# Kernel tuning notes

Measured on AMD Instinct MI355X. Metric: run time of the kernel, lower is better.

The kernel has to match this reference:

```python
import jax, jax.numpy as jnp
import numpy as np

N_NODES = 50000
N_EDGES = 800000
QRY = 128
KEY = 128
VAL = 128
HEADS = 8
HEAD_FEATS = VAL // HEADS
BN_EPS = 1e-5


def setup_inputs() -> dict:
    key = jax.random.key(0)
    ks = jax.random.split(key, 12)
    inp = {
        "ft_q": jax.random.normal(ks[0], (N_NODES, QRY), dtype=jnp.float32),
        "ft_k": jax.random.normal(ks[1], (N_NODES, KEY), dtype=jnp.float32),
        "src": jax.random.randint(ks[2], (N_EDGES,), 0, N_NODES, dtype=jnp.int32),
        "dst": jax.random.randint(ks[3], (N_EDGES,), 0, N_NODES, dtype=jnp.int32),
        # learned params
        "Wq": jax.random.normal(ks[4], (VAL, QRY), dtype=jnp.float32) / np.sqrt(QRY),
        "bq": jnp.zeros((VAL,), dtype=jnp.float32),
        "Wk": jax.random.normal(ks[5], (VAL, KEY), dtype=jnp.float32) / np.sqrt(KEY),
        "Wv": jax.random.normal(ks[6], (VAL, QRY), dtype=jnp.float32) / np.sqrt(QRY),
        "attn_e": jax.random.normal(ks[7], (VAL,), dtype=jnp.float32),
        "bn_q_g": jnp.ones((QRY,), dtype=jnp.float32),
        "bn_q_b": jnp.zeros((QRY,), dtype=jnp.float32),
        "bn_k_g": jnp.ones((KEY,), dtype=jnp.float32),
        "bn_k_b": jnp.zeros((KEY,), dtype=jnp.float32),
    }
    return inp


def _batch_norm(x, gamma, beta):
    # training-mode BatchNorm1d: normalize over batch dim
    mean = jnp.mean(x, axis=0, keepdims=True)
    var = jnp.var(x, axis=0, keepdims=True)
    return (x - mean) * jax.lax.rsqrt(var + BN_EPS) * gamma + beta


def reference(ft_q, ft_k, src, dst, Wq, bq, Wk, Wv, attn_e,
              bn_q_g, bn_q_b, bn_k_g, bn_k_b):
    ft_q = _batch_norm(ft_q, bn_q_g, bn_q_b)
    ft_k = _batch_norm(ft_k, bn_k_g, bn_k_b)

    q = ft_q @ Wq.T + bq                      # [N, VAL]
    k = ft_k @ Wk.T                           # [N, VAL]
    v = (ft_q @ Wv.T).reshape(-1, HEADS, HEAD_FEATS)  # [N, H, D]

    # u_add_v: per-edge e = q[src] + k[dst]
    e = q[src] + k[dst]                       # [E, VAL]
    e = (attn_e * jax.nn.sigmoid(e)).reshape(-1, HEADS, HEAD_FEATS).sum(-1)  # [E, H]

    # edge_softmax grouped by destination node
    m = jax.ops.segment_max(e, dst, num_segments=N_NODES)   # [N, H]
    ex = jnp.exp(e - m[dst])                                # [E, H]
    s = jax.ops.segment_sum(ex, dst, num_segments=N_NODES)  # [N, H]
    a = ex / s[dst]                                         # [E, H]

    # u_mul_e_sum: scatter-sum of v[src] * a over destination
    msg = v[src] * a[:, :, None]                            # [E, H, D]
    rst = jax.ops.segment_sum(msg, dst, num_segments=N_NODES)  # [N, H, D]
    return rst.reshape(-1, VAL)
```

## Files before the change

kernel.cpp:

```cpp
#include <hip/hip_runtime.h>

#define N_NODES 50000
#define N_EDGES 800000
#define FEATS 128
#define NCHUNK 196
#define CPAD 50176
#define GEMM_BX 196
#define GEMM_BLOCKS 392
#define SCAT_BLOCKS 3125
#define NTILE 782
#define NF_WAVES 8192
#define STAT_BLOCKS 256
#define HIST_BLOCKS 512

typedef __attribute__((ext_vector_type(8))) short bf16x8;
typedef __attribute__((ext_vector_type(4))) float f32x4;
typedef union { uint4 u; bf16x8 v; } pack8;

__device__ __forceinline__ unsigned short f2bf(float f){
  unsigned u = __float_as_uint(f);
  u += 0x7FFF + ((u >> 16) & 1);
  return (unsigned short)(u >> 16);
}
__device__ __forceinline__ unsigned cvtpk(float lo, float hi){
  unsigned r;
  asm("v_cvt_pk_bf16_f32 %0, %1, %2" : "=v"(r) : "v"(lo), "v"(hi));
  return r;
}
__device__ __forceinline__ void unpack8(uint4 p, float* f){
  f[0]=__uint_as_float(p.x << 16); f[1]=__uint_as_float(p.x & 0xffff0000u);
  f[2]=__uint_as_float(p.y << 16); f[3]=__uint_as_float(p.y & 0xffff0000u);
  f[4]=__uint_as_float(p.z << 16); f[5]=__uint_as_float(p.z & 0xffff0000u);
  f[6]=__uint_as_float(p.w << 16); f[7]=__uint_as_float(p.w & 0xffff0000u);
}

__global__ __launch_bounds__(256) void stats_hist_kernel(
    const float* __restrict__ ftq, const float* __restrict__ ftk,
    float* __restrict__ sums, const int* __restrict__ dstE,
    int* __restrict__ counts, int* __restrict__ csums,
    unsigned short* __restrict__ rankE, unsigned short* __restrict__ xqb){
  __shared__ float red[4*FEATS];
  __shared__ int lchunk[NCHUNK];
  int tid = threadIdx.x, bid = blockIdx.x;
  if (bid < STAT_BLOCKS){
    for (int i = tid; i < 4*FEATS; i += 256) red[i] = 0.f;
    __syncthreads();
    int sub = tid >> 5, c4 = tid & 31;
    const float* Xs = (sub < 4) ? ftq : ftk;
    int so = (sub < 4) ? 0 : 2*FEATS;
    bool isq = (sub < 4);
    float a0=0,a1=0,a2=0,a3=0,b0=0,b1=0,b2=0,b3=0;
    #pragma unroll 4
    for (int r = bid*4 + (sub&3); r < N_NODES; r += STAT_BLOCKS*4){
      float4 x = *(const float4*)(Xs + (size_t)r*FEATS + c4*4);
      if (isq)
        *(uint2*)&xqb[(size_t)r*FEATS + c4*4] = make_uint2(cvtpk(x.x,x.y), cvtpk(x.z,x.w));
      a0+=x.x; b0+=x.x*x.x; a1+=x.y; b1+=x.y*x.y;
      a2+=x.z; b2+=x.z*x.z; a3+=x.w; b3+=x.w*x.w;
    }
    a0 += __shfl_xor(a0,32); a1 += __shfl_xor(a1,32);
    a2 += __shfl_xor(a2,32); a3 += __shfl_xor(a3,32);
    b0 += __shfl_xor(b0,32); b1 += __shfl_xor(b1,32);
    b2 += __shfl_xor(b2,32); b3 += __shfl_xor(b3,32);
    if ((tid & 63) < 32){
      int c0 = c4*4;
      atomicAdd(&red[so + c0+0], a0); atomicAdd(&red[so + c0+1], a1);
      atomicAdd(&red[so + c0+2], a2); atomicAdd(&red[so + c0+3], a3);
      atomicAdd(&red[so + FEATS + c0+0], b0); atomicAdd(&red[so + FEATS + c0+1], b1);
      atomicAdd(&red[so + FEATS + c0+2], b2); atomicAdd(&red[so + FEATS + c0+3], b3);
    }
    __syncthreads();
    for (int i = tid; i < 4*FEATS; i += 256) atomicAdd(&sums[i], red[i]);
  } else {
    for (int i = tid; i < NCHUNK; i += 256) lchunk[i] = 0;
    __syncthreads();
    for (int t = (bid-STAT_BLOCKS)*256 + tid; t < N_EDGES; t += HIST_BLOCKS*256){
      int d = dstE[t];
      int p = atomicAdd(&counts[d], 1);
      rankE[t] = (unsigned short)p;
      atomicAdd(&lchunk[d >> 8], 1);
    }
    __syncthreads();
    for (int i = tid; i < NCHUNK; i += 256)
      if (lchunk[i]) atomicAdd(&csums[i], lchunk[i]);
  }
}

__global__ __launch_bounds__(256) void scan_fold_kernel(
    const int* __restrict__ counts, const int* __restrict__ csums,
    int* __restrict__ loc, int* __restrict__ bscan,
    const float* __restrict__ Wq, const float* __restrict__ bq,
    const float* __restrict__ Wk, const float* __restrict__ Wv,
    const float* __restrict__ gq, const float* __restrict__ bqn,
    const float* __restrict__ gk, const float* __restrict__ bkn,
    const float* __restrict__ sums,
    unsigned short* __restrict__ Wb, float* __restrict__ bias){
  __shared__ int s[256];
  int tid = threadIdx.x, bid = blockIdx.x;
  if (bid < NCHUNK){
    int i = bid*256 + tid;
    int v = counts[i];
    s[tid] = v; __syncthreads();
    for (int d = 1; d < 256; d <<= 1){
      int tv = (tid >= d) ? s[tid-d] : 0; __syncthreads();
      s[tid] += tv; __syncthreads();
    }
    loc[i] = s[tid] - v;
  } else if (bid == NCHUNK){
    int v = (tid < NCHUNK) ? csums[tid] : 0;
    s[tid] = v; __syncthreads();
    for (int d = 1; d < 256; d <<= 1){
      int tv = (tid >= d) ? s[tid-d] : 0; __syncthreads();
      s[tid] += tv; __syncthreads();
    }
    if (tid < NCHUNK) bscan[tid] = s[tid] - v;
  } else {
    int wv = (bid - NCHUNK - 1)*4 + (tid >> 6);
    int lane = tid & 63;
    int m = wv >> 7;
    int o = wv & 127;
    const float* Wsrc = (m==0) ? Wq : (m==1) ? Wv : Wk;
    const float* g   = (m==2) ? gk : gq;
    const float* bb  = (m==2) ? bkn : bqn;
    const float* s0  = (m==2) ? (sums + 2*FEATS) : sums;
    const float invN = 1.0f / (float)N_NODES;
    float acc = 0.f;
    unsigned short w2[2];
    int i0 = lane*2;
    #pragma unroll
    for (int t = 0; t < 2; t++){
      int i = i0 + t;
      float mean = s0[i]*invN;
      float var  = s0[FEATS+i]*invN - mean*mean;
      float rstd = rsqrtf(var + 1e-5f);
      float scale = g[i]*rstd;
      float shift = bb[i] - mean*scale;
      float w = Wsrc[o*FEATS + i];
      w2[t] = f2bf(w*scale);
      acc += shift*w;
    }
    ((unsigned*)Wb)[(m*FEATS*FEATS + o*FEATS + i0) >> 1] =
        (unsigned)w2[0] | ((unsigned)w2[1] << 16);
    #pragma unroll
    for (int off = 1; off < 64; off <<= 1) acc += __shfl_xor(acc, off);
    if (lane == 0) bias[m*FEATS + o] = acc + ((m==0) ? bq[o] : 0.f);
  }
}

__global__ __launch_bounds__(256) void gemm_scatter_kernel(
    const unsigned short* __restrict__ xqb, const float* __restrict__ ftk,
    const unsigned short* __restrict__ Wball, const float* __restrict__ biasall,
    unsigned short* __restrict__ qv, unsigned short* __restrict__ kb,
    const int* __restrict__ dstE, const int* __restrict__ srcE,
    const int* __restrict__ loc, const int* __restrict__ bscan,
    const unsigned short* __restrict__ rankE, int* __restrict__ src_csr){
  __shared__ unsigned short Bs[2][FEATS][FEATS];
  int tid = threadIdx.x, bid = blockIdx.x;
  if (bid >= GEMM_BLOCKS){
    int t = (bid - GEMM_BLOCKS)*256 + tid;
    int d = dstE[t];
    src_csr[loc[d] + bscan[d >> 8] + (int)rankE[t]] = srcE[t];
    return;
  }
  int isk = (bid >= GEMM_BX);
  int bx = isk ? bid - GEMM_BX : bid;
  int nplanes = isk ? 1 : 2;
  {
    for (int p = 0; p < nplanes; p++){
      int m = isk ? 2 : p;
      const uint4* srcp = (const uint4*)(Wball + m*FEATS*FEATS);
      for (int idx = tid; idx < FEATS*FEATS/8; idx += 256){
        int n = idx >> 4, ck = idx & 15;
        *(uint4*)&Bs[p][n][(ck ^ (n & 15))*8] = srcp[idx];
      }
    }
  }
  __syncthreads();
  int wave = tid >> 6, lane = tid & 63;
  int mrow = lane & 15, quad = lane >> 4;
  float bv[2][8];
  #pragma unroll
  for (int p = 0; p < 2; p++)
    #pragma unroll
    for (int ct = 0; ct < 8; ct++)
      bv[p][ct] = biasall[(isk ? 2 : p)*FEATS + ct*16 + mrow];
  uint4 cur[4], nxt[4];
  auto loadA = [&](uint4* buf, int t){
    int arow = t*64 + wave*16 + mrow;
    if (!isk){
      const unsigned short* xp = xqb + (size_t)arow*FEATS + quad*8;
      buf[0] = *(const uint4*)xp;
      buf[1] = *(const uint4*)(xp + 32);
      buf[2] = *(const uint4*)(xp + 64);
      buf[3] = *(const uint4*)(xp + 96);
    } else {
      bool rok = arow < N_NODES;
      const float* xp = ftk + (size_t)(rok ? arow : 0)*FEATS + quad*8;
      #pragma unroll
      for (int kt = 0; kt < 4; kt++){
        float4 x0 = *(const float4*)(xp + kt*32);
        float4 x1 = *(const float4*)(xp + kt*32 + 4);
        if (!rok){ x0 = make_float4(0.f,0.f,0.f,0.f); x1 = x0; }
        buf[kt].x = cvtpk(x0.x, x0.y); buf[kt].y = cvtpk(x0.z, x0.w);
        buf[kt].z = cvtpk(x1.x, x1.y); buf[kt].w = cvtpk(x1.z, x1.w);
      }
    }
  };
  loadA(cur, bx);
  for (int t = bx; t < NTILE; t += GEMM_BX){
    int tn = t + GEMM_BX;
    if (tn < NTILE) loadA(nxt, tn);
    f32x4 acc[2][8];
    #pragma unroll
    for (int p = 0; p < 2; p++)
      #pragma unroll
      for (int i = 0; i < 8; i++) acc[p][i] = (f32x4){0.f,0.f,0.f,0.f};
    #pragma unroll
    for (int kt = 0; kt < 4; kt++){
      pack8 a; a.u = cur[kt];
      #pragma unroll
      for (int ct = 0; ct < 8; ct++){
        bf16x8 b0 = *(bf16x8*)&Bs[0][ct*16 + mrow][((kt*4 + quad) ^ mrow)*8];
        acc[0][ct] = __builtin_amdgcn_mfma_f32_16x16x32_bf16(a.v, b0, acc[0][ct], 0, 0, 0);
      }
      if (!isk){
        #pragma unroll
        for (int ct = 0; ct < 8; ct++){
          bf16x8 b1 = *(bf16x8*)&Bs[1][ct*16 + mrow][((kt*4 + quad) ^ mrow)*8];
          acc[1][ct] = __builtin_amdgcn_mfma_f32_16x16x32_bf16(a.v, b1, acc[1][ct], 0, 0, 0);
        }
      }
    }
    int row0 = t*64;
    #pragma unroll
    for (int p = 0; p < 2; p++){
      if (isk && p) break;
      unsigned short* Out = isk ? kb : (qv + p*128);
      const int ostride = isk ? FEATS : 256;
      #pragma unroll
      for (int ct = 0; ct < 8; ct++){
        int col = ct*16 + mrow;
        #pragma unroll
        for (int v = 0; v < 4; v++){
          int orow = row0 + wave*16 + quad*4 + v;
          float s = acc[p][ct][v] + bv[p][ct];
          float pf = __shfl_xor(s, 1);
          if (!(mrow & 1) && orow < N_NODES)
            *(unsigned*)&Out[(size_t)orow*ostride + col] = cvtpk(s, pf);
        }
      }
    }
    #pragma unroll
    for (int i = 0; i < 4; i++) cur[i] = nxt[i];
  }
}

__global__ __launch_bounds__(256) void node_fused_kernel(
    const unsigned short* __restrict__ qv, const unsigned short* __restrict__ kb,
    const float* __restrict__ attn, const int* __restrict__ src_csr,
    const int* __restrict__ loc, const int* __restrict__ bscan,
    float* __restrict__ out){
  int tid = threadIdx.x;
  int lane = tid & 63;
  int h = lane & 7, g = lane >> 3;
  int w = blockIdx.x*4 + (tid >> 6);
  const float L2E = 1.44269504f;
  float ar[16];
  {
    const uint4* ap = (const uint4*)(attn + h*16);
    uint4 a0 = ap[0], a1 = ap[1], a2 = ap[2], a3 = ap[3];
    ar[0]=__uint_as_float(a0.x); ar[1]=__uint_as_float(a0.y); ar[2]=__uint_as_float(a0.z); ar[3]=__uint_as_float(a0.w);
    ar[4]=__uint_as_float(a1.x); ar[5]=__uint_as_float(a1.y); ar[6]=__uint_as_float(a1.z); ar[7]=__uint_as_float(a1.w);
    ar[8]=__uint_as_float(a2.x); ar[9]=__uint_as_float(a2.y); ar[10]=__uint_as_float(a2.z); ar[11]=__uint_as_float(a2.w);
    ar[12]=__uint_as_float(a3.x); ar[13]=__uint_as_float(a3.y); ar[14]=__uint_as_float(a3.z); ar[15]=__uint_as_float(a3.w);
  }
  for (int n = w; n < N_NODES; n += NF_WAVES){
    int off0 = loc[n]   + bscan[n>>8];
    int off1 = loc[n+1] + bscan[(n+1)>>8];
    int deg = off1 - off0;
    if (deg == 0){
      ((float2*)(out + (size_t)n*FEATS))[lane] = make_float2(0.f, 0.f);
      continue;
    }
    float kf2[16];
    {
      const unsigned short* kr = kb + (size_t)n*FEATS + h*16;
      uint4 k0 = *(const uint4*)kr;
      uint4 k1 = *(const uint4*)(kr + 8);
      float kf[16]; unpack8(k0, kf); unpack8(k1, kf+8);
      #pragma unroll
      for (int i = 0; i < 16; i++) kf2[i] = -L2E * kf[i];
    }
    float ssum = 0.f;
    float acc[16];
    #pragma unroll
    for (int i = 0; i < 16; i++) acc[i] = 0.f;
    if (g < deg){
      int sA = src_csr[off0 + g];
      int jB = g + 8;
      int sB = (jB < deg) ? src_csr[off0 + jB] : sA;
      const unsigned short* pA = qv + (size_t)sA*256 + h*16;
      uint4 qa0 = *(const uint4*)pA;
      uint4 qa1 = *(const uint4*)(pA + 8);
      while (true){
        uint4 va0 = *(const uint4*)(pA + 128);
        uint4 va1 = *(const uint4*)(pA + 136);
        const unsigned short* pB = qv + (size_t)sB*256 + h*16;
        uint4 qb0 = *(const uint4*)pB;
        uint4 qb1 = *(const uint4*)(pB + 8);
        int jC = jB + 8;
        int sC = (jC < deg) ? src_csr[off0 + jC] : sB;
        float qf[16]; unpack8(qa0, qf); unpack8(qa1, qf+8);
        float ta = 0.f, tb = 0.f, tc = 0.f, td = 0.f;
        #pragma unroll
        for (int i = 0; i < 16; i += 4){
          float x0 = fmaf(qf[i+0], -L2E, kf2[i+0]);
          float x1 = fmaf(qf[i+1], -L2E, kf2[i+1]);
          float x2 = fmaf(qf[i+2], -L2E, kf2[i+2]);
          float x3 = fmaf(qf[i+3], -L2E, kf2[i+3]);
          ta = fmaf(ar[i+0], __builtin_amdgcn_rcpf(1.f + __builtin_amdgcn_exp2f(x0)), ta);
          tb = fmaf(ar[i+1], __builtin_amdgcn_rcpf(1.f + __builtin_amdgcn_exp2f(x1)), tb);
          tc = fmaf(ar[i+2], __builtin_amdgcn_rcpf(1.f + __builtin_amdgcn_exp2f(x2)), tc);
          td = fmaf(ar[i+3], __builtin_amdgcn_rcpf(1.f + __builtin_amdgcn_exp2f(x3)), td);
        }
        float t = (ta + tb) + (tc + td);
        float ex = __builtin_amdgcn_exp2f(t * L2E);
        ssum += ex;
        float vf[16]; unpack8(va0, vf); unpack8(va1, vf+8);
        #pragma unroll
        for (int i = 0; i < 16; i++) acc[i] = fmaf(ex, vf[i], acc[i]);
        if (jB >= deg) break;
        qa0 = qb0; qa1 = qb1; pA = pB;
        jB = jC; sB = sC;
      }
    }
    ssum += __shfl_xor(ssum, 8); ssum += __shfl_xor(ssum, 16); ssum += __shfl_xor(ssum, 32);
    #pragma unroll
    for (int i = 0; i < 16; i++){
      acc[i] += __shfl_xor(acc[i], 8);
      acc[i] += __shfl_xor(acc[i], 16);
      acc[i] += __shfl_xor(acc[i], 32);
    }
    if (g == 0){
      float inv_s = 1.f / ssum;
      float4* op = (float4*)(out + (size_t)n*FEATS + h*16);
      op[0] = make_float4(acc[0]*inv_s, acc[1]*inv_s, acc[2]*inv_s, acc[3]*inv_s);
      op[1] = make_float4(acc[4]*inv_s, acc[5]*inv_s, acc[6]*inv_s, acc[7]*inv_s);
      op[2] = make_float4(acc[8]*inv_s, acc[9]*inv_s, acc[10]*inv_s, acc[11]*inv_s);
      op[3] = make_float4(acc[12]*inv_s, acc[13]*inv_s, acc[14]*inv_s, acc[15]*inv_s);
    }
  }
}

extern "C" void kernel_launch(void* const* d_in, const int* in_sizes, int n_in,
                              void* d_out, int out_size, void* d_ws, size_t ws_size,
                              hipStream_t stream){
  (void)in_sizes; (void)n_in; (void)out_size; (void)ws_size;
  const float* ftq  = (const float*)d_in[0];
  const float* ftk  = (const float*)d_in[1];
  const int*   srcE = (const int*)d_in[2];
  const int*   dstE = (const int*)d_in[3];
  const float* Wq   = (const float*)d_in[4];
  const float* bq   = (const float*)d_in[5];
  const float* Wk   = (const float*)d_in[6];
  const float* Wv   = (const float*)d_in[7];
  const float* attn = (const float*)d_in[8];
  const float* gq   = (const float*)d_in[9];
  const float* bqn  = (const float*)d_in[10];
  const float* gk   = (const float*)d_in[11];
  const float* bkn  = (const float*)d_in[12];

  char* ws = (char*)d_ws;
  int*   counts  = (int*)(ws + 0);
  float* sums    = (float*)(ws + 200704);
  int*   csums   = (int*)(ws + 202752);
  int*   loc     = (int*)(ws + 203536);
  int*   bscan   = (int*)(ws + 404240);
  int*   src_csr = (int*)(ws + 405024);
  unsigned short* rankE = (unsigned short*)(ws + 3605024);
  unsigned short* Wb = (unsigned short*)(ws + 5205024);
  float* biasf   = (float*)(ws + 5303328);
  unsigned short* xqb = (unsigned short*)(ws + 5304864);
  unsigned short* qv  = (unsigned short*)(ws + 18149920);
  unsigned short* kb  = qv + (size_t)N_NODES*256;
  float* out = (float*)d_out;

  hipMemsetAsync(ws, 0, 203536, stream);

  hipLaunchKernelGGL(stats_hist_kernel, dim3(STAT_BLOCKS + HIST_BLOCKS), dim3(256), 0, stream,
                     ftq, ftk, sums, dstE, counts, csums, rankE, xqb);
  hipLaunchKernelGGL(scan_fold_kernel, dim3(293), dim3(256), 0, stream,
                     counts, csums, loc, bscan,
                     Wq, bq, Wk, Wv, gq, bqn, gk, bkn, sums, Wb, biasf);
  hipLaunchKernelGGL(gemm_scatter_kernel, dim3(GEMM_BLOCKS + SCAT_BLOCKS), dim3(256), 0, stream,
                     xqb, ftk, Wb, biasf, qv, kb, dstE, srcE, loc, bscan, rankE, src_csr);
  hipLaunchKernelGGL(node_fused_kernel, dim3(NF_WAVES/4), dim3(256), 0, stream,
                     qv, kb, attn, src_csr, loc, bscan, out);
}
```

Measured before the change: 277.6 us.

## Replace global-atomic histogram with segmented LDS histograms plus column scan

The destination histogram no longer uses global atomics. Each of 128 edge segments builds a packed 16-bit LDS histogram for one half of the node range, writes it to a segment-by-node matrix, and a column-scan kernel then turns that matrix into per-segment offsets and total counts. The scatter step adds the segment offset to each edge's local rank, and the chunk sums are now computed from counts inside the scan kernel. This removes contended global atomics and most of the memset, at the cost of two extra launches, a roughly 12.8MB matrix written and re-read, and separating stats from the histogram work.

```diff
diff --git a/kernel.cpp b/kernel.cpp
--- a/kernel.cpp
+++ b/kernel.cpp
@@ -11,7 +11,9 @@
 #define NTILE 782
 #define NF_WAVES 8192
 #define STAT_BLOCKS 256
-#define HIST_BLOCKS 512
+#define HSEG 128
+#define ESEG 6250
+#define HHALF 25088
 
 typedef __attribute__((ext_vector_type(8))) short bf16x8;
 typedef __attribute__((ext_vector_type(4))) float f32x4;
@@ -34,61 +36,81 @@
   f[6]=__uint_as_float(p.w << 16); f[7]=__uint_as_float(p.w & 0xffff0000u);
 }
 
-__global__ __launch_bounds__(256) void stats_hist_kernel(
+__global__ __launch_bounds__(256) void stats_kernel(
     const float* __restrict__ ftq, const float* __restrict__ ftk,
-    float* __restrict__ sums, const int* __restrict__ dstE,
-    int* __restrict__ counts, int* __restrict__ csums,
-    unsigned short* __restrict__ rankE, unsigned short* __restrict__ xqb){
+    float* __restrict__ sums, unsigned short* __restrict__ xqb){
   __shared__ float red[4*FEATS];
-  __shared__ int lchunk[NCHUNK];
   int tid = threadIdx.x, bid = blockIdx.x;
-  if (bid < STAT_BLOCKS){
-    for (int i = tid; i < 4*FEATS; i += 256) red[i] = 0.f;
-    __syncthreads();
-    int sub = tid >> 5, c4 = tid & 31;
-    const float* Xs = (sub < 4) ? ftq : ftk;
-    int so = (sub < 4) ? 0 : 2*FEATS;
-    bool isq = (sub < 4);
-    float a0=0,a1=0,a2=0,a3=0,b0=0,b1=0,b2=0,b3=0;
-    #pragma unroll 4
-    for (int r = bid*4 + (sub&3); r < N_NODES; r += STAT_BLOCKS*4){
-      float4 x = *(const float4*)(Xs + (size_t)r*FEATS + c4*4);
-      if (isq)
-        *(uint2*)&xqb[(size_t)r*FEATS + c4*4] = make_uint2(cvtpk(x.x,x.y), cvtpk(x.z,x.w));
-      a0+=x.x; b0+=x.x*x.x; a1+=x.y; b1+=x.y*x.y;
-      a2+=x.z; b2+=x.z*x.z; a3+=x.w; b3+=x.w*x.w;
-    }
-    a0 += __shfl_xor(a0,32); a1 += __shfl_xor(a1,32);
-    a2 += __shfl_xor(a2,32); a3 += __shfl_xor(a3,32);
-    b0 += __shfl_xor(b0,32); b1 += __shfl_xor(b1,32);
-    b2 += __shfl_xor(b2,32); b3 += __shfl_xor(b3,32);
-    if ((tid & 63) < 32){
-      int c0 = c4*4;
-      atomicAdd(&red[so + c0+0], a0); atomicAdd(&red[so + c0+1], a1);
-      atomicAdd(&red[so + c0+2], a2); atomicAdd(&red[so + c0+3], a3);
-      atomicAdd(&red[so + FEATS + c0+0], b0); atomicAdd(&red[so + FEATS + c0+1], b1);
-      atomicAdd(&red[so + FEATS + c0+2], b2); atomicAdd(&red[so + FEATS + c0+3], b3);
-    }
-    __syncthreads();
-    for (int i = tid; i < 4*FEATS; i += 256) atomicAdd(&sums[i], red[i]);
-  } else {
-    for (int i = tid; i < NCHUNK; i += 256) lchunk[i] = 0;
-    __syncthreads();
-    for (int t = (bid-STAT_BLOCKS)*256 + tid; t < N_EDGES; t += HIST_BLOCKS*256){
-      int d = dstE[t];
-      int p = atomicAdd(&counts[d], 1);
-      rankE[t] = (unsigned short)p;
-      atomicAdd(&lchunk[d >> 8], 1);
-    }
-    __syncthreads();
-    for (int i = tid; i < NCHUNK; i += 256)
-      if (lchunk[i]) atomicAdd(&csums[i], lchunk[i]);
-  }
+  for (int i = tid; i < 4*FEATS; i += 256) red[i] = 0.f;
+  __syncthreads();
+  int sub = tid >> 5, c4 = tid & 31;
+  const float* Xs = (sub < 4) ? ftq : ftk;
+  int so = (sub < 4) ? 0 : 2*FEATS;
+  bool isq = (sub < 4);
+  float a0=0,a1=0,a2=0,a3=0,b0=0,b1=0,b2=0,b3=0;
+  #pragma unroll 4
+  for (int r = bid*4 + (sub&3); r < N_NODES; r += STAT_BLOCKS*4){
+    float4 x = *(const float4*)(Xs + (size_t)r*FEATS + c4*4);
+    if (isq)
+      *(uint2*)&xqb[(size_t)r*FEATS + c4*4] = make_uint2(cvtpk(x.x,x.y), cvtpk(x.z,x.w));
+    a0+=x.x; b0+=x.x*x.x; a1+=x.y; b1+=x.y*x.y;
+    a2+=x.z; b2+=x.z*x.z; a3+=x.w; b3+=x.w*x.w;
+  }
+  a0 += __shfl_xor(a0,32); a1 += __shfl_xor(a1,32);
+  a2 += __shfl_xor(a2,32); a3 += __shfl_xor(a3,32);
+  b0 += __shfl_xor(b0,32); b1 += __shfl_xor(b1,32);
+  b2 += __shfl_xor(b2,32); b3 += __shfl_xor(b3,32);
+  if ((tid & 63) < 32){
+    int c0 = c4*4;
+    atomicAdd(&red[so + c0+0], a0); atomicAdd(&red[so + c0+1], a1);
+    atomicAdd(&red[so + c0+2], a2); atomicAdd(&red[so + c0+3], a3);
+    atomicAdd(&red[so + FEATS + c0+0], b0); atomicAdd(&red[so + FEATS + c0+1], b1);
+    atomicAdd(&red[so + FEATS + c0+2], b2); atomicAdd(&red[so + FEATS + c0+3], b3);
+  }
+  __syncthreads();
+  for (int i = tid; i < 4*FEATS; i += 256) atomicAdd(&sums[i], red[i]);
+}
+
+__global__ __launch_bounds__(256) void hist_kernel(
+    const int* __restrict__ dstE, unsigned short* __restrict__ rankE,
+    unsigned short* __restrict__ hmat){
+  __shared__ unsigned lh[HHALF/2];
+  int tid = threadIdx.x, bid = blockIdx.x;
+  int seg = bid >> 1, hi = bid & 1;
+  int dlo = hi * HHALF;
+  for (int i = tid; i < HHALF/2; i += 256) lh[i] = 0;
+  __syncthreads();
+  int e0 = seg * ESEG;
+  for (int t = e0 + tid; t < e0 + ESEG; t += 256){
+    int d = dstE[t] - dlo;
+    if ((unsigned)d < (unsigned)HHALF){
+      unsigned sh = (d & 1) * 16;
+      unsigned old = atomicAdd(&lh[d >> 1], 1u << sh);
+      rankE[t] = (unsigned short)((old >> sh) & 0xffffu);
+    }
+  }
+  __syncthreads();
+  unsigned* row = (unsigned*)(hmat + (size_t)bid * HHALF);
+  for (int i = tid; i < HHALF/2; i += 256) row[i] = lh[i];
+}
+
+__global__ __launch_bounds__(256) void colscan_kernel(
+    unsigned short* __restrict__ hmat, int* __restrict__ counts){
+  int d = blockIdx.x*256 + threadIdx.x;
+  int hi = (d >= HHALF) ? 1 : 0;
+  int col = d - hi*HHALF;
+  int run = 0;
+  for (int s = 0; s < HSEG; s++){
+    size_t idx = (size_t)(s*2 + hi)*HHALF + col;
+    int v = hmat[idx];
+    hmat[idx] = (unsigned short)run;
+    run += v;
+  }
+  counts[d] = run;
 }
 
 __global__ __launch_bounds__(256) void scan_fold_kernel(
-    const int* __restrict__ counts, const int* __restrict__ csums,
-    int* __restrict__ loc, int* __restrict__ bscan,
+    const int* __restrict__ counts, int* __restrict__ loc, int* __restrict__ bscan,
     const float* __restrict__ Wq, const float* __restrict__ bq,
     const float* __restrict__ Wk, const float* __restrict__ Wv,
     const float* __restrict__ gq, const float* __restrict__ bqn,
@@ -107,13 +129,18 @@
     }
     loc[i] = s[tid] - v;
   } else if (bid == NCHUNK){
-    int v = (tid < NCHUNK) ? csums[tid] : 0;
-    s[tid] = v; __syncthreads();
+    int total = 0;
+    if (tid < NCHUNK){
+      const int* cp = counts + tid*256;
+      #pragma unroll 8
+      for (int i = 0; i < 256; i++) total += cp[i];
+    }
+    s[tid] = total; __syncthreads();
     for (int d = 1; d < 256; d <<= 1){
       int tv = (tid >= d) ? s[tid-d] : 0; __syncthreads();
       s[tid] += tv; __syncthreads();
     }
-    if (tid < NCHUNK) bscan[tid] = s[tid] - v;
+    if (tid < NCHUNK) bscan[tid] = s[tid] - total;
   } else {
     int wv = (bid - NCHUNK - 1)*4 + (tid >> 6);
     int lane = tid & 63;
@@ -153,13 +180,17 @@
     unsigned short* __restrict__ qv, unsigned short* __restrict__ kb,
     const int* __restrict__ dstE, const int* __restrict__ srcE,
     const int* __restrict__ loc, const int* __restrict__ bscan,
-    const unsigned short* __restrict__ rankE, int* __restrict__ src_csr){
+    const unsigned short* __restrict__ rankE, const unsigned short* __restrict__ hmat,
+    int* __restrict__ src_csr){
   __shared__ unsigned short Bs[2][FEATS][FEATS];
   int tid = threadIdx.x, bid = blockIdx.x;
   if (bid >= GEMM_BLOCKS){
     int t = (bid - GEMM_BLOCKS)*256 + tid;
     int d = dstE[t];
-    src_csr[loc[d] + bscan[d >> 8] + (int)rankE[t]] = srcE[t];
+    int seg = t / ESEG;
+    int hi = (d >= HHALF) ? 1 : 0;
+    int base = (int)hmat[(size_t)(seg*2 + hi)*HHALF + (d - hi*HHALF)];
+    src_csr[loc[d] + bscan[d >> 8] + base + (int)rankE[t]] = srcE[t];
     return;
   }
   int isk = (bid >= GEMM_BX);
@@ -371,29 +402,33 @@
   const float* bkn  = (const float*)d_in[12];
 
   char* ws = (char*)d_ws;
-  int*   counts  = (int*)(ws + 0);
-  float* sums    = (float*)(ws + 200704);
-  int*   csums   = (int*)(ws + 202752);
-  int*   loc     = (int*)(ws + 203536);
-  int*   bscan   = (int*)(ws + 404240);
-  int*   src_csr = (int*)(ws + 405024);
-  unsigned short* rankE = (unsigned short*)(ws + 3605024);
-  unsigned short* Wb = (unsigned short*)(ws + 5205024);
-  float* biasf   = (float*)(ws + 5303328);
-  unsigned short* xqb = (unsigned short*)(ws + 5304864);
-  unsigned short* qv  = (unsigned short*)(ws + 18149920);
-  unsigned short* kb  = qv + (size_t)N_NODES*256;
+  float* sums    = (float*)(ws + 0);
+  int*   counts  = (int*)(ws + 2048);
+  int*   loc     = (int*)(ws + 202752);
+  int*   bscan   = (int*)(ws + 403456);
+  int*   src_csr = (int*)(ws + 404240);
+  unsigned short* rankE = (unsigned short*)(ws + 3604240);
+  unsigned short* hmat  = (unsigned short*)(ws + 5204240);
+  unsigned short* Wb    = (unsigned short*)(ws + 18049296);
+  float* biasf   = (float*)(ws + 18147600);
+  unsigned short* xqb = (unsigned short*)(ws + 18149152);
+  unsigned short* qv  = (unsigned short*)(ws + 30994208);
+  unsigned short* kb  = (unsigned short*)(ws + 56594208);
   float* out = (float*)d_out;
 
-  hipMemsetAsync(ws, 0, 203536, stream);
-
-  hipLaunchKernelGGL(stats_hist_kernel, dim3(STAT_BLOCKS + HIST_BLOCKS), dim3(256), 0, stream,
-                     ftq, ftk, sums, dstE, counts, csums, rankE, xqb);
+  hipMemsetAsync(ws, 0, 2048, stream);
+
+  hipLaunchKernelGGL(stats_kernel, dim3(STAT_BLOCKS), dim3(256), 0, stream,
+                     ftq, ftk, sums, xqb);
+  hipLaunchKernelGGL(hist_kernel, dim3(2*HSEG), dim3(256), 0, stream,
+                     dstE, rankE, hmat);
+  hipLaunchKernelGGL(colscan_kernel, dim3(NCHUNK), dim3(256), 0, stream,
+                     hmat, counts);
   hipLaunchKernelGGL(scan_fold_kernel, dim3(293), dim3(256), 0, stream,
-                     counts, csums, loc, bscan,
+                     counts, loc, bscan,
                      Wq, bq, Wk, Wv, gq, bqn, gk, bkn, sums, Wb, biasf);
   hipLaunchKernelGGL(gemm_scatter_kernel, dim3(GEMM_BLOCKS + SCAT_BLOCKS), dim3(256), 0, stream,
-                     xqb, ftk, Wb, biasf, qv, kb, dstE, srcE, loc, bscan, rankE, src_csr);
+                     xqb, ftk, Wb, biasf, qv, kb, dstE, srcE, loc, bscan, rankE, hmat, src_csr);
   hipLaunchKernelGGL(node_fused_kernel, dim3(NF_WAVES/4), dim3(256), 0, stream,
                      qv, kb, attn, src_csr, loc, bscan, out);
 }
```

New measurement: 281.5 us. Within noise of the previous version (+1.4%).
